# Kernel optimization log

Measured on AMD Instinct MI355X. Metric: run time of the kernel, lower is better.

## Reference

```python
import jax, jax.numpy as jnp
import numpy as np

H = 512   # hidden_size
E = 256   # embed_size / listener feature dim
V = 34    # vocab
EPS = 1e-12  # F.normalize(p=1) eps


def setup_inputs() -> dict:
    k = jax.random.key(0)
    ks = jax.random.split(k, 12)
    S, B, T = 512, 512, 160
    def n(kk, shape, s=0.05):
        return jax.random.normal(kk, shape, jnp.float32) * s
    return {
        "key": n(ks[0], (S, B, E), 1.0),
        "value": n(ks[1], (S, B, E), 1.0),
        "mask": jnp.ones((B, S), jnp.float32),
        "labels": jax.random.randint(ks[2], (B, T), 0, V),
        "Wq": n(ks[3], (E, H)), "bq": jnp.zeros((E,), jnp.float32),
        "Wsc": n(ks[4], (V, E + H)), "bsc": jnp.zeros((V,), jnp.float32),
        "Emb": n(ks[5], (V, E), 1.0),
        "Wih0": n(ks[6], (4 * H, H)), "Whh0": n(ks[7], (4 * H, H)),
        "bih0": jnp.zeros((4 * H,), jnp.float32), "bhh0": jnp.zeros((4 * H,), jnp.float32),
        "Wih1": n(ks[8], (4 * H, H)), "Whh1": n(ks[9], (4 * H, H)),
        "bih1": jnp.zeros((4 * H,), jnp.float32), "bhh1": jnp.zeros((4 * H,), jnp.float32),
        "s0": jnp.zeros((H,), jnp.float32), "s1": jnp.zeros((H,), jnp.float32),
        "cs0": jnp.zeros((H,), jnp.float32), "cs1": jnp.zeros((H,), jnp.float32),
    }


def _lstm_cell(x, h, c, Wih, Whh, bih, bhh):
    g = x @ Wih.T + bih + h @ Whh.T + bhh          # (B, 4H)
    i, f, gg, o = jnp.split(g, 4, axis=1)          # torch gate order i,f,g,o
    c2 = jax.nn.sigmoid(f) * c + jax.nn.sigmoid(i) * jnp.tanh(gg)
    h2 = jax.nn.sigmoid(o) * jnp.tanh(c2)
    return h2, c2


def reference(key, value, mask, labels, Wq, bq, Wsc, bsc, Emb,
              Wih0, Whh0, bih0, bhh0, Wih1, Whh1, bih1, bhh1,
              s0, s1, cs0, cs1):
    kT = jnp.transpose(key, (1, 0, 2))    # (B, S, E)
    vT = jnp.transpose(value, (1, 0, 2))  # (B, S, E)
    lab = labels.T                        # (T, B)
    embeds = Emb[lab]                     # (T, B, E)
    B = kT.shape[0]

    h0 = jnp.broadcast_to(s0, (B, H))
    h1 = jnp.broadcast_to(s1, (B, H))
    c0 = jnp.broadcast_to(cs0, (B, H))
    c1 = jnp.broadcast_to(cs1, (B, H))

    def attend(h):
        q = h @ Wq.T + bq                               # (B, E)
        e = jax.nn.softmax(jnp.einsum('bse,be->bs', kT, q), axis=1)
        e = e * mask
        alpha = e / jnp.maximum(jnp.sum(e, axis=1, keepdims=True), EPS)
        return jnp.einsum('bs,bse->be', alpha, vT)      # context (B, E)

    # step 0: attention + first cell updates, no scoring output
    ctx = attend(h1)
    inp = jnp.concatenate([embeds[0], ctx], axis=1)
    h0, c0 = _lstm_cell(inp, h0, c0, Wih0, Whh0, bih0, bhh0)
    h1, c1 = _lstm_cell(h0, h1, c1, Wih1, Whh1, bih1, bhh1)

    def step(carry, emb_i):
        h0, c0, h1, c1 = carry
        ctx = attend(h1)
        out = jnp.concatenate([h1, ctx], axis=1) @ Wsc.T + bsc  # (B, V)
        inp = jnp.concatenate([emb_i, ctx], axis=1)             # teacher forcing
        h0n, c0n = _lstm_cell(inp, h0, c0, Wih0, Whh0, bih0, bhh0)
        h1n, c1n = _lstm_cell(h0n, h1, c1, Wih1, Whh1, bih1, bhh1)
        return (h0n, c0n, h1n, c1n), out

    (h0, c0, h1, c1), outs = jax.lax.scan(step, (h0, c0, h1, c1), embeds[1:])

    ctx = attend(h1)
    out_last = jnp.concatenate([h1, ctx], axis=1) @ Wsc.T + bsc
    y = jnp.concatenate([outs, out_last[None]], axis=0)  # (T, B, V)
    return jnp.transpose(y, (1, 0, 2))                   # (B, T, V)
```

## Files before the change

kernel.cpp:

```cpp
#include <hip/hip_runtime.h>
#include <hip/hip_bf16.h>
#include <cstdint>
#include <cstddef>

#define S_LEN 512
#define B_SZ  512
#define T_LEN 160
#define E_DIM 256
#define H_DIM 512
#define V_DIM 34
#define G4    2048
#define XROW  768
#define EPS1  1e-12f
#define BE    (B_SZ * E_DIM)

typedef unsigned short u16;
typedef unsigned char  u8;
typedef __attribute__((ext_vector_type(8))) short bf16x8;
typedef __attribute__((ext_vector_type(4))) float f32x4;

#define SMEM_BYTES 18432

__device__ __forceinline__ float wave_reduce_sum(float v) {
#pragma unroll
  for (int m = 32; m >= 1; m >>= 1) v += __shfl_xor(v, m, 64);
  return v;
}
__device__ __forceinline__ float half_reduce_sum(float v) {
#pragma unroll
  for (int m = 16; m >= 1; m >>= 1) v += __shfl_xor(v, m, 64);
  return v;
}
__device__ __forceinline__ float wave_reduce_max(float v) {
#pragma unroll
  for (int m = 32; m >= 1; m >>= 1) v = fmaxf(v, __shfl_xor(v, m, 64));
  return v;
}
__device__ __forceinline__ float bf2f(u16 u) {
  return __uint_as_float((uint32_t)u << 16);
}
__device__ __forceinline__ float4 loadV4(const u8* p) {
  uint32_t u = *(const uint32_t*)p;
  float4 r;
  r.x = __builtin_amdgcn_cvt_f32_fp8(u, 0);
  r.y = __builtin_amdgcn_cvt_f32_fp8(u, 1);
  r.z = __builtin_amdgcn_cvt_f32_fp8(u, 2);
  r.w = __builtin_amdgcn_cvt_f32_fp8(u, 3);
  return r;
}
__device__ __forceinline__ float4 loadV4(const float* p) { return *(const float4*)p; }

__device__ __forceinline__ float dot8(const u16* p, const float* q) {
  bf16x8 k8 = *(const bf16x8*)p;
  float acc = 0.f;
#pragma unroll
  for (int i = 0; i < 8; ++i) acc += bf2f((u16)k8[i]) * q[i];
  return acc;
}
__device__ __forceinline__ float dot8(const float* p, const float* q) {
  float4 a = *(const float4*)p, b = *(const float4*)(p + 4);
  return a.x*q[0] + a.y*q[1] + a.z*q[2] + a.w*q[3] +
         b.x*q[4] + b.y*q[5] + b.z*q[6] + b.w*q[7];
}
__device__ __forceinline__ u16 f2bf(float f) {
  uint32_t u = __float_as_uint(f);
  uint32_t r = (u + 0x7FFFu + ((u >> 16) & 1u)) >> 16;
  return (u16)r;
}
__device__ __forceinline__ float sigm(float x) { return 1.f / (1.f + __expf(-x)); }

__device__ __forceinline__ void mfma_acc(const u16* A, int lda, const u16* W, int ldw,
                                         int klen, int m0, int n0, char* smem,
                                         f32x4 (&acc)[2][2]) {
  u16 (*As)[72] = (u16(*)[72])smem;
  u16 (*Ws)[72] = (u16(*)[72])(smem + 64 * 72 * 2);
  const int tid = threadIdx.x;
  const int lane = tid & 63, wave = tid >> 6;
  const int wm = (wave >> 1) * 32, wn = (wave & 1) * 32;
  const int row = lane & 15, kq = (lane >> 4) * 8;

  for (int k0 = 0; k0 < klen; k0 += 64) {
    __syncthreads();
#pragma unroll
    for (int i = tid; i < 512; i += 256) {
      int r = i >> 3, c = (i & 7) * 8;
      *(bf16x8*)&As[r][c] = *(const bf16x8*)(A + (size_t)(m0 + r) * lda + k0 + c);
      *(bf16x8*)&Ws[r][c] = *(const bf16x8*)(W + (size_t)(n0 + r) * ldw + k0 + c);
    }
    __syncthreads();
#pragma unroll
    for (int kk = 0; kk < 64; kk += 32) {
      bf16x8 a0 = *(const bf16x8*)&As[wm + row][kk + kq];
      bf16x8 a1 = *(const bf16x8*)&As[wm + 16 + row][kk + kq];
      bf16x8 b0 = *(const bf16x8*)&Ws[wn + row][kk + kq];
      bf16x8 b1 = *(const bf16x8*)&Ws[wn + 16 + row][kk + kq];
      acc[0][0] = __builtin_amdgcn_mfma_f32_16x16x32_bf16(a0, b0, acc[0][0], 0, 0, 0);
      acc[0][1] = __builtin_amdgcn_mfma_f32_16x16x32_bf16(a0, b1, acc[0][1], 0, 0, 0);
      acc[1][0] = __builtin_amdgcn_mfma_f32_16x16x32_bf16(a1, b0, acc[1][0], 0, 0, 0);
      acc[1][1] = __builtin_amdgcn_mfma_f32_16x16x32_bf16(a1, b1, acc[1][1], 0, 0, 0);
    }
  }
}

__global__ __launch_bounds__(256)
void init_state(const float* __restrict__ s0, const float* __restrict__ s1,
                const float* __restrict__ cs0, const float* __restrict__ cs1,
                u16* __restrict__ h0b, u16* __restrict__ h1b,
                float* __restrict__ c0, float* __restrict__ c1) {
  int idx = blockIdx.x * blockDim.x + threadIdx.x;
  int j = idx & 511;
  h0b[idx] = f2bf(s0[j]);
  h1b[idx] = f2bf(s1[j]);
  c0[idx] = cs0[j];
  c1[idx] = cs1[j];
}

__global__ __launch_bounds__(256)
void conv_bf16(const float* __restrict__ in, u16* __restrict__ outp, int n4) {
  int i = blockIdx.x * blockDim.x + threadIdx.x;
  int stride = gridDim.x * blockDim.x;
  for (; i < n4; i += stride) {
    float4 f = ((const float4*)in)[i];
    ushort4 u;
    u.x = f2bf(f.x); u.y = f2bf(f.y); u.z = f2bf(f.z); u.w = f2bf(f.w);
    ((ushort4*)outp)[i] = u;
  }
}

__global__ __launch_bounds__(256)
void conv_fp8(const float* __restrict__ in, u8* __restrict__ outp, int n4) {
  int i = blockIdx.x * blockDim.x + threadIdx.x;
  int stride = gridDim.x * blockDim.x;
  for (; i < n4; i += stride) {
    float4 f = ((const float4*)in)[i];
    uint32_t packed = 0;
    packed = __builtin_amdgcn_cvt_pk_fp8_f32(f.x, f.y, packed, false);
    packed = __builtin_amdgcn_cvt_pk_fp8_f32(f.z, f.w, packed, true);
    ((uint32_t*)outp)[i] = packed;
  }
}

__global__ __launch_bounds__(256)
void pack_w(const float* __restrict__ in, u16* __restrict__ outp) {
  int idx = blockIdx.x * 256 + threadIdx.x;
  int k = (idx & 63) * 8;
  int np = idx >> 6;
  int j = np >> 2, g = np & 3;
  const float* src = in + ((size_t)(g * 512 + j)) * 512 + k;
  float4 f0 = *(const float4*)src;
  float4 f1 = *(const float4*)(src + 4);
  ushort4 o0, o1;
  o0.x = f2bf(f0.x); o0.y = f2bf(f0.y); o0.z = f2bf(f0.z); o0.w = f2bf(f0.w);
  o1.x = f2bf(f1.x); o1.y = f2bf(f1.y); o1.z = f2bf(f1.z); o1.w = f2bf(f1.w);
  *(ushort4*)(outp + (size_t)np * 512 + k) = o0;
  *(ushort4*)(outp + (size_t)np * 512 + k + 4) = o1;
}

__global__ __launch_bounds__(256)
void pack_wq(const float* __restrict__ in, u16* __restrict__ outp) {
  int idx = blockIdx.x * 256 + threadIdx.x;
  int k = (idx & 63) * 8;
  int e = idx >> 6;
  const float* src = in + (size_t)e * 512 + k;
  float4 f0 = *(const float4*)src;
  float4 f1 = *(const float4*)(src + 4);
  ushort4 o0, o1;
  o0.x = f2bf(f0.x); o0.y = f2bf(f0.y); o0.z = f2bf(f0.z); o0.w = f2bf(f0.w);
  o1.x = f2bf(f1.x); o1.y = f2bf(f1.y); o1.z = f2bf(f1.z); o1.w = f2bf(f1.w);
  *(ushort4*)(outp + (size_t)e * 512 + k) = o0;
  *(ushort4*)(outp + (size_t)e * 512 + k + 4) = o1;
}

__global__ __launch_bounds__(256)
void pack_wsc(const float* __restrict__ in, u16* __restrict__ outp) {
  int idx = blockIdx.x * 256 + threadIdx.x;
  if (idx >= 64 * 96) return;
  int kq = (idx % 96) * 8;
  int v = idx / 96;
  ushort4 o0 = {0, 0, 0, 0}, o1 = {0, 0, 0, 0};
  if (v < V_DIM) {
    const float* src = in + (size_t)v * XROW + kq;
    float4 f0 = *(const float4*)src;
    float4 f1 = *(const float4*)(src + 4);
    o0.x = f2bf(f0.x); o0.y = f2bf(f0.y); o0.z = f2bf(f0.z); o0.w = f2bf(f0.w);
    o1.x = f2bf(f1.x); o1.y = f2bf(f1.y); o1.z = f2bf(f1.z); o1.w = f2bf(f1.w);
  }
  *(ushort4*)(outp + (size_t)v * XROW + kq) = o0;
  *(ushort4*)(outp + (size_t)v * XROW + kq + 4) = o1;
}

__global__ __launch_bounds__(256)
void pack_bias(const float* bih0, const float* bhh0,
               const float* bih1, const float* bhh1,
               float* bias0p, float* bias1p) {
  int np = blockIdx.x * 256 + threadIdx.x;
  int j = np >> 2, g = np & 3;
  int n = g * 512 + j;
  bias0p[np] = bih0[n] + bhh0[n];
  bias1p[np] = bih1[n] + bhh1[n];
}

__global__ __launch_bounds__(256)
void gather_embs(const float* __restrict__ Emb, const int* __restrict__ labels,
                 u16* __restrict__ embs) {
  int idx = blockIdx.x * 256 + threadIdx.x;
  if (idx >= T_LEN * B_SZ * 64) return;
  int q = idx & 63;
  int b = (idx >> 6) & 511;
  int t = idx >> 15;
  int lab = labels[(size_t)b * T_LEN + t];
  float4 f = *(const float4*)(Emb + (size_t)lab * E_DIM + q * 4);
  ushort4 o;
  o.x = f2bf(f.x); o.y = f2bf(f.y); o.z = f2bf(f.z); o.w = f2bf(f.w);
  *(ushort4*)(embs + ((size_t)t * B_SZ + b) * E_DIM + q * 4) = o;
}

__global__ __launch_bounds__(256)
void qgemm(const u16* __restrict__ h1b, const u16* __restrict__ Wqb,
           const float* __restrict__ bq, float* __restrict__ qbuf) {
  __shared__ char smem[SMEM_BYTES];
  const int lane = threadIdx.x & 63, wave = threadIdx.x >> 6;
  const int m0 = blockIdx.y * 64, n0 = blockIdx.x * 64;
  f32x4 acc[2][2] = {};
  mfma_acc(h1b, H_DIM, Wqb, 512, 512, m0, n0, smem, acc);
  const int wm = (wave >> 1) * 32, wn = (wave & 1) * 32;
  const int col = lane & 15, r4 = (lane >> 4) * 4;
#pragma unroll
  for (int fm = 0; fm < 2; ++fm)
#pragma unroll
    for (int fn = 0; fn < 2; ++fn) {
      int cc = n0 + wn + fn * 16 + col;
      float bias = bq[cc];
#pragma unroll
      for (int r = 0; r < 4; ++r) {
        int rr = m0 + wm + fm * 16 + r4 + r;
        qbuf[(size_t)rr * E_DIM + cc] = acc[fm][fn][r] + bias;
      }
    }
}

template <typename KT, typename VT, bool DEFER>
__global__ __launch_bounds__(256)
void fusedA(const KT* __restrict__ key, const VT* __restrict__ value,
            const float* __restrict__ mask, const float* __restrict__ qbuf,
            const float* __restrict__ Wsc, const float* __restrict__ bsc,
            const u16* __restrict__ embs,
            const u16* __restrict__ h0b, const u16* __restrict__ h1b,
            const u16* __restrict__ Wih0p, const u16* __restrict__ Whh0p,
            const u16* __restrict__ Whh1p,
            u16* __restrict__ xc0, u16* __restrict__ xhist,
            float* __restrict__ pg0, float* __restrict__ pg1,
            float* __restrict__ out, int t) {
  __shared__ char smem[SMEM_BYTES];
  const int tid = threadIdx.x;
  const int lane = tid & 63;
  const int wave = tid >> 6;

  if (blockIdx.x >= 512) {
    if (t >= T_LEN) return;
    int gb = blockIdx.x - 512;
    int m0 = ((gb & 255) >> 5) * 64, n0 = (gb & 31) * 64;
    f32x4 acc[2][2] = {};
    float* pg;
    if (gb < 256) {
      mfma_acc(h0b, H_DIM, Whh0p, 512, 512, m0, n0, smem, acc);
      mfma_acc(embs + (size_t)t * BE, E_DIM, Wih0p, 512, 256, m0, n0, smem, acc);
      pg = pg0;
    } else {
      mfma_acc(h1b, H_DIM, Whh1p, 512, 512, m0, n0, smem, acc);
      pg = pg1;
    }
    const int wm = (wave >> 1) * 32, wn = (wave & 1) * 32;
    const int col = lane & 15, r4 = (lane >> 4) * 4;
#pragma unroll
    for (int fm = 0; fm < 2; ++fm)
#pragma unroll
      for (int fn = 0; fn < 2; ++fn) {
        int cc = n0 + wn + fn * 16 + col;
#pragma unroll
        for (int r = 0; r < 4; ++r) {
          int rr = m0 + wm + fm * 16 + r4 + r;
          pg[(size_t)rr * G4 + cc] = acc[fm][fn][r];
        }
      }
    return;
  }

  float* qs   = (float*)smem;
  float* scb  = qs + 256;
  float* ctxs = scb + 512;
  float* ctxp = ctxs + 256;
  float* red  = ctxp + 1024;
  float* h1s  = red + 8;
  const int b = blockIdx.x;

  qs[tid] = qbuf[(size_t)b * E_DIM + tid];
  if (!DEFER) {
#pragma unroll
    for (int j = tid; j < H_DIM; j += 256) h1s[j] = bf2f(h1b[(size_t)b * H_DIM + j]);
  }
  __syncthreads();

  {
    int e0 = (lane & 31) << 3;
    float q8[8];
    *(float4*)&q8[0] = *(const float4*)&qs[e0];
    *(float4*)&q8[4] = *(const float4*)&qs[e0 + 4];
    int s = wave * 4 + (lane >> 5) * 2;
    const KT* kp = key + (size_t)s * BE + (size_t)b * E_DIM + e0;
#pragma unroll 4
    for (int it = 0; it < 32; ++it) {
      float a0 = dot8(kp, q8);
      float a1 = dot8(kp + BE, q8);
      a0 = half_reduce_sum(a0);
      a1 = half_reduce_sum(a1);
      if ((lane & 31) == 0) { scb[s] = a0; scb[s + 1] = a1; }
      s += 16;
      kp += (size_t)16 * BE;
    }
  }
  __syncthreads();

  float v0 = scb[tid], v1 = scb[tid + 256];
  {
    float lm = wave_reduce_max(fmaxf(v0, v1));
    if (lane == 0) red[wave] = lm;
  }
  __syncthreads();
  float smax = fmaxf(fmaxf(red[0], red[1]), fmaxf(red[2], red[3]));
  __syncthreads();
  float m0 = mask[(size_t)b * S_LEN + tid];
  float m1 = mask[(size_t)b * S_LEN + tid + 256];
  float p0 = __expf(v0 - smax), p1 = __expf(v1 - smax);
  float pm0 = p0 * m0, pm1 = p1 * m1;
  {
    float sP = wave_reduce_sum(p0 + p1);
    float sPM = wave_reduce_sum(pm0 + pm1);
    if (lane == 0) { red[wave] = sP; red[4 + wave] = sPM; }
  }
  __syncthreads();
  float P  = red[0] + red[1] + red[2] + red[3];
  float PM = red[4] + red[5] + red[6] + red[7];
  float inv = 1.f / fmaxf(PM, EPS1 * P);
  scb[tid] = pm0 * inv;
  scb[tid + 256] = pm1 * inv;
  __syncthreads();

  {
    float4 cacc = {0.f, 0.f, 0.f, 0.f};
    const VT* vp = value + (size_t)wave * BE + (size_t)b * E_DIM + (lane << 2);
#pragma unroll 16
    for (int s = wave; s < S_LEN; s += 4) {
      float a = scb[s];
      float4 v4 = loadV4(vp);
      cacc.x += a * v4.x; cacc.y += a * v4.y; cacc.z += a * v4.z; cacc.w += a * v4.w;
      vp += (size_t)4 * BE;
    }
    *(float4*)&ctxp[wave * 256 + (lane << 2)] = cacc;
  }
  __syncthreads();
  {
    float ctxe = ctxp[tid] + ctxp[256 + tid] + ctxp[512 + tid] + ctxp[768 + tid];
    ctxs[tid] = ctxe;
    u16 cb = f2bf(ctxe);
    if (t < T_LEN) xc0[(size_t)b * E_DIM + tid] = cb;
    if (DEFER && t >= 1) xhist[((size_t)t * B_SZ + b) * XROW + H_DIM + tid] = cb;
  }

  if (!DEFER) {
    __syncthreads();
    if (t >= 1) {
      for (int v = wave; v < V_DIM; v += 4) {
        const float4* wr = reinterpret_cast<const float4*>(Wsc + (size_t)v * XROW);
        float4 w0 = wr[lane];
        float4 w1 = wr[lane + 64];
        float4 w2 = wr[lane + 128];
        const float* ha = &h1s[4 * lane];
        const float* hb = &h1s[256 + 4 * lane];
        const float* cx = &ctxs[4 * lane];
        float acc = w0.x * ha[0] + w0.y * ha[1] + w0.z * ha[2] + w0.w * ha[3] +
                    w1.x * hb[0] + w1.y * hb[1] + w1.z * hb[2] + w1.w * hb[3] +
                    w2.x * cx[0] + w2.y * cx[1] + w2.z * cx[2] + w2.w * cx[3];
        acc = wave_reduce_sum(acc);
        if (lane == 0) out[((size_t)b * T_LEN + (t - 1)) * V_DIM + v] = acc + bsc[v];
      }
    }
  }
}

__global__ __launch_bounds__(256)
void cell_kernel(const u16* __restrict__ A, int lda, const u16* __restrict__ Wp,
                 int klen,
                 const float* __restrict__ pg, const float* __restrict__ biasp,
                 float* __restrict__ cbuf,
                 u16* __restrict__ hb, u16* __restrict__ xh) {
  __shared__ char smem[SMEM_BYTES];
  const int tid = threadIdx.x;
  const int lane = tid & 63, wave = tid >> 6;
  const int m0 = blockIdx.y * 64, n0 = blockIdx.x * 64;

  f32x4 acc[2][2] = {};
  mfma_acc(A, lda, Wp, 512, klen, m0, n0, smem, acc);
  __syncthreads();

  float (*Cs)[68] = (float(*)[68])smem;
  const int wm = (wave >> 1) * 32, wn = (wave & 1) * 32;
  const int col = lane & 15, r4 = (lane >> 4) * 4;
#pragma unroll
  for (int fm = 0; fm < 2; ++fm)
#pragma unroll
    for (int fn = 0; fn < 2; ++fn) {
      int cc = wn + fn * 16 + col;
      float bias = biasp[n0 + cc];
#pragma unroll
      for (int r = 0; r < 4; ++r) {
        int rr = wm + fm * 16 + r4 + r;
        Cs[rr][cc] = acc[fm][fn][r] + pg[(size_t)(m0 + rr) * G4 + n0 + cc] + bias;
      }
    }
  __syncthreads();

  for (int i = tid; i < 1024; i += 256) {
    int m = i >> 4, j = i & 15;
    float4 gv = *(const float4*)&Cs[m][j * 4];
    float ii = sigm(gv.x), ff = sigm(gv.y), tg = tanhf(gv.z), oo = sigm(gv.w);
    int gm = m0 + m, gj = (n0 >> 2) + j;
    size_t cidx = (size_t)gm * H_DIM + gj;
    float cn = ff * cbuf[cidx] + ii * tg;
    float hn = oo * tanhf(cn);
    cbuf[cidx] = cn;
    u16 hv = f2bf(hn);
    hb[cidx] = hv;
    if (xh) xh[(size_t)gm * XROW + gj] = hv;
  }
}

__global__ __launch_bounds__(256)
void score_kernel(const u16* __restrict__ xhist, const u16* __restrict__ Wscb,
                  const float* __restrict__ bsc, float* __restrict__ out) {
  __shared__ char smem[SMEM_BYTES];
  const int tau = blockIdx.x + 1;
  const int m0 = blockIdx.y * 64;
  const int lane = threadIdx.x & 63, wave = threadIdx.x >> 6;
  f32x4 acc[2][2] = {};
  mfma_acc(xhist + (size_t)tau * B_SZ * XROW, XROW, Wscb, XROW, XROW, m0, 0, smem, acc);
  const int wm = (wave >> 1) * 32, wn = (wave & 1) * 32;
  const int col = lane & 15, r4 = (lane >> 4) * 4;
#pragma unroll
  for (int fm = 0; fm < 2; ++fm)
#pragma unroll
    for (int fn = 0; fn < 2; ++fn) {
      int cc = wn + fn * 16 + col;
      if (cc >= V_DIM) continue;
      float bias = bsc[cc];
#pragma unroll
      for (int r = 0; r < 4; ++r) {
        int b = m0 + wm + fm * 16 + r4 + r;
        out[((size_t)b * T_LEN + (tau - 1)) * V_DIM + cc] = acc[fm][fn][r] + bias;
      }
    }
}

extern "C" void kernel_launch(void* const* d_in, const int* in_sizes, int n_in,
                              void* d_out, int out_size, void* d_ws, size_t ws_size,
                              hipStream_t stream) {
  (void)in_sizes; (void)n_in; (void)out_size;

  const float* key    = (const float*)d_in[0];
  const float* value  = (const float*)d_in[1];
  const float* mask   = (const float*)d_in[2];
  const int*   labels = (const int*)d_in[3];
  const float* Wq     = (const float*)d_in[4];
  const float* bq     = (const float*)d_in[5];
  const float* Wsc    = (const float*)d_in[6];
  const float* bsc    = (const float*)d_in[7];
  const float* Emb    = (const float*)d_in[8];
  const float* Wih0   = (const float*)d_in[9];
  const float* Whh0   = (const float*)d_in[10];
  const float* bih0   = (const float*)d_in[11];
  const float* bhh0   = (const float*)d_in[12];
  const float* Wih1   = (const float*)d_in[13];
  const float* Whh1   = (const float*)d_in[14];
  const float* bih1   = (const float*)d_in[15];
  const float* bhh1   = (const float*)d_in[16];
  const float* s0     = (const float*)d_in[17];
  const float* s1     = (const float*)d_in[18];
  const float* cs0    = (const float*)d_in[19];
  const float* cs1    = (const float*)d_in[20];
  float* out = (float*)d_out;

  char* ws = (char*)d_ws;
  size_t off = 0;
  auto alloc = [&](size_t bytes) -> void* {
    void* p = ws + off;
    off += (bytes + 255) & ~(size_t)255;
    return p;
  };
  u16*   h0b    = (u16*)alloc((size_t)B_SZ * H_DIM * 2);
  u16*   h1b    = (u16*)alloc((size_t)B_SZ * H_DIM * 2);
  float* c0     = (float*)alloc((size_t)B_SZ * H_DIM * 4);
  float* c1     = (float*)alloc((size_t)B_SZ * H_DIM * 4);
  u16*   xc0    = (u16*)alloc((size_t)B_SZ * E_DIM * 2);
  float* qbuf   = (float*)alloc((size_t)B_SZ * E_DIM * 4);
  float* pg0    = (float*)alloc((size_t)B_SZ * G4 * 4);
  float* pg1    = (float*)alloc((size_t)B_SZ * G4 * 4);
  u16*   Wih0p  = (u16*)alloc((size_t)G4 * 512 * 2);
  u16*   Whh0p  = (u16*)alloc((size_t)G4 * 512 * 2);
  u16*   Wih1p  = (u16*)alloc((size_t)G4 * 512 * 2);
  u16*   Whh1p  = (u16*)alloc((size_t)G4 * 512 * 2);
  u16*   Wqb    = (u16*)alloc((size_t)E_DIM * 512 * 2);
  u16*   Wscb   = (u16*)alloc((size_t)64 * XROW * 2);
  float* bias0p = (float*)alloc((size_t)G4 * 4);
  float* bias1p = (float*)alloc((size_t)G4 * 4);
  u16*   embs   = (u16*)alloc((size_t)T_LEN * B_SZ * E_DIM * 2);

  const size_t kv_elems = (size_t)S_LEN * B_SZ * E_DIM;
  bool lowkv = (ws_size >= off + kv_elems * 2 + kv_elems + 1024);
  u16* kb = nullptr; u8* vb = nullptr;
  if (lowkv) {
    kb = (u16*)alloc(kv_elems * 2);
    vb = (u8*)alloc(kv_elems);
  }
  const size_t xh_bytes = (size_t)(T_LEN + 1) * B_SZ * XROW * 2;
  bool defer = (ws_size >= off + xh_bytes + 1024);
  u16* xhist = nullptr;
  if (defer) xhist = (u16*)alloc(xh_bytes);

  init_state<<<(B_SZ * H_DIM) / 256, 256, 0, stream>>>(s0, s1, cs0, cs1, h0b, h1b, c0, c1);
  pack_w<<<512, 256, 0, stream>>>(Wih0, Wih0p);
  pack_w<<<512, 256, 0, stream>>>(Whh0, Whh0p);
  pack_w<<<512, 256, 0, stream>>>(Wih1, Wih1p);
  pack_w<<<512, 256, 0, stream>>>(Whh1, Whh1p);
  pack_wq<<<64, 256, 0, stream>>>(Wq, Wqb);
  if (defer) pack_wsc<<<24, 256, 0, stream>>>(Wsc, Wscb);
  pack_bias<<<8, 256, 0, stream>>>(bih0, bhh0, bih1, bhh1, bias0p, bias1p);
  gather_embs<<<(T_LEN * B_SZ * 64 + 255) / 256, 256, 0, stream>>>(Emb, labels, embs);

  if (lowkv) {
    int n4 = (int)(kv_elems / 4);
    conv_bf16<<<4096, 256, 0, stream>>>(key, kb, n4);
    conv_fp8<<<4096, 256, 0, stream>>>(value, vb, n4);
  }

  dim3 qgrid(E_DIM / 64, B_SZ / 64);
  qgemm<<<qgrid, 256, 0, stream>>>(h1b, Wqb, bq, qbuf);

  dim3 cell_grid(G4 / 64, B_SZ / 64);
  for (int t = 0; t <= T_LEN; ++t) {
    if (lowkv) {
      if (defer)
        fusedA<u16, u8, true><<<1024, 256, 0, stream>>>(
            kb, vb, mask, qbuf, Wsc, bsc, embs, h0b, h1b,
            Wih0p, Whh0p, Whh1p, xc0, xhist, pg0, pg1, out, t);
      else
        fusedA<u16, u8, false><<<1024, 256, 0, stream>>>(
            kb, vb, mask, qbuf, Wsc, bsc, embs, h0b, h1b,
            Wih0p, Whh0p, Whh1p, xc0, xhist, pg0, pg1, out, t);
    } else {
      if (defer)
        fusedA<float, float, true><<<1024, 256, 0, stream>>>(
            key, value, mask, qbuf, Wsc, bsc, embs, h0b, h1b,
            Wih0p, Whh0p, Whh1p, xc0, xhist, pg0, pg1, out, t);
      else
        fusedA<float, float, false><<<1024, 256, 0, stream>>>(
            key, value, mask, qbuf, Wsc, bsc, embs, h0b, h1b,
            Wih0p, Whh0p, Whh1p, xc0, xhist, pg0, pg1, out, t);
    }
    if (t < T_LEN) {
      cell_kernel<<<cell_grid, 256, 0, stream>>>(
          xc0, E_DIM, Wih0p + 256, 256, pg0, bias0p, c0, h0b, nullptr);
      cell_kernel<<<cell_grid, 256, 0, stream>>>(
          h0b, H_DIM, Wih1p, 512, pg1, bias1p, c1, h1b,
          defer ? xhist + (size_t)(t + 1) * B_SZ * XROW : nullptr);
      qgemm<<<qgrid, 256, 0, stream>>>(h1b, Wqb, bq, qbuf);
    }
  }

  if (defer) {
    dim3 sgrid(T_LEN, B_SZ / 64);
    score_kernel<<<sgrid, 256, 0, stream>>>(xhist, Wscb, bsc, out);
  }
}
```

Before: 10.86 ms.

## Load MFMA operands directly from global memory, dropping LDS staging and barriers

Replaces the shared-memory-tiled MFMA helper with one that loads bf16 fragments straight from global memory into registers, removing LDS stores and __syncthreads from every GEMM (qgemm, fusedA gate GEMMs, cell_kernel, score_kernel). Shared memory is now declared per kernel at its actual size, which may raise occupancy. The attention score loop is also restructured to process four sequence positions per iteration instead of two, for more loads in flight. The cost is that each wave now reads its operands from global memory or cache rather than sharing tiles through LDS, which raises L2 traffic and makes the loads less coalesced.

```diff
diff --git a/kernel.cpp b/kernel.cpp
--- a/kernel.cpp
+++ b/kernel.cpp
@@ -19,8 +19,6 @@
 typedef __attribute__((ext_vector_type(8))) short bf16x8;
 typedef __attribute__((ext_vector_type(4))) float f32x4;
 
-#define SMEM_BYTES 18432
-
 __device__ __forceinline__ float wave_reduce_sum(float v) {
 #pragma unroll
   for (int m = 32; m >= 1; m >>= 1) v += __shfl_xor(v, m, 64);
@@ -69,36 +67,26 @@
 }
 __device__ __forceinline__ float sigm(float x) { return 1.f / (1.f + __expf(-x)); }
 
-__device__ __forceinline__ void mfma_acc(const u16* A, int lda, const u16* W, int ldw,
-                                         int klen, int m0, int n0, char* smem,
-                                         f32x4 (&acc)[2][2]) {
-  u16 (*As)[72] = (u16(*)[72])smem;
-  u16 (*Ws)[72] = (u16(*)[72])(smem + 64 * 72 * 2);
-  const int tid = threadIdx.x;
-  const int lane = tid & 63, wave = tid >> 6;
+__device__ __forceinline__ void mfma_direct(const u16* A, int lda, const u16* W, int ldw,
+                                            int klen, int m0, int n0,
+                                            f32x4 (&acc)[2][2]) {
+  const int lane = threadIdx.x & 63, wave = threadIdx.x >> 6;
   const int wm = (wave >> 1) * 32, wn = (wave & 1) * 32;
   const int row = lane & 15, kq = (lane >> 4) * 8;
-
-  for (int k0 = 0; k0 < klen; k0 += 64) {
-    __syncthreads();
-#pragma unroll
-    for (int i = tid; i < 512; i += 256) {
-      int r = i >> 3, c = (i & 7) * 8;
-      *(bf16x8*)&As[r][c] = *(const bf16x8*)(A + (size_t)(m0 + r) * lda + k0 + c);
-      *(bf16x8*)&Ws[r][c] = *(const bf16x8*)(W + (size_t)(n0 + r) * ldw + k0 + c);
-    }
-    __syncthreads();
-#pragma unroll
-    for (int kk = 0; kk < 64; kk += 32) {
-      bf16x8 a0 = *(const bf16x8*)&As[wm + row][kk + kq];
-      bf16x8 a1 = *(const bf16x8*)&As[wm + 16 + row][kk + kq];
-      bf16x8 b0 = *(const bf16x8*)&Ws[wn + row][kk + kq];
-      bf16x8 b1 = *(const bf16x8*)&Ws[wn + 16 + row][kk + kq];
-      acc[0][0] = __builtin_amdgcn_mfma_f32_16x16x32_bf16(a0, b0, acc[0][0], 0, 0, 0);
-      acc[0][1] = __builtin_amdgcn_mfma_f32_16x16x32_bf16(a0, b1, acc[0][1], 0, 0, 0);
-      acc[1][0] = __builtin_amdgcn_mfma_f32_16x16x32_bf16(a1, b0, acc[1][0], 0, 0, 0);
-      acc[1][1] = __builtin_amdgcn_mfma_f32_16x16x32_bf16(a1, b1, acc[1][1], 0, 0, 0);
-    }
+  const u16* a0p = A + (size_t)(m0 + wm + row) * lda + kq;
+  const u16* a1p = A + (size_t)(m0 + wm + 16 + row) * lda + kq;
+  const u16* b0p = W + (size_t)(n0 + wn + row) * ldw + kq;
+  const u16* b1p = W + (size_t)(n0 + wn + 16 + row) * ldw + kq;
+#pragma unroll 4
+  for (int k = 0; k < klen; k += 32) {
+    bf16x8 a0 = *(const bf16x8*)(a0p + k);
+    bf16x8 a1 = *(const bf16x8*)(a1p + k);
+    bf16x8 b0 = *(const bf16x8*)(b0p + k);
+    bf16x8 b1 = *(const bf16x8*)(b1p + k);
+    acc[0][0] = __builtin_amdgcn_mfma_f32_16x16x32_bf16(a0, b0, acc[0][0], 0, 0, 0);
+    acc[0][1] = __builtin_amdgcn_mfma_f32_16x16x32_bf16(a0, b1, acc[0][1], 0, 0, 0);
+    acc[1][0] = __builtin_amdgcn_mfma_f32_16x16x32_bf16(a1, b0, acc[1][0], 0, 0, 0);
+    acc[1][1] = __builtin_amdgcn_mfma_f32_16x16x32_bf16(a1, b1, acc[1][1], 0, 0, 0);
   }
 }
 
@@ -218,11 +206,10 @@
 __global__ __launch_bounds__(256)
 void qgemm(const u16* __restrict__ h1b, const u16* __restrict__ Wqb,
            const float* __restrict__ bq, float* __restrict__ qbuf) {
-  __shared__ char smem[SMEM_BYTES];
   const int lane = threadIdx.x & 63, wave = threadIdx.x >> 6;
   const int m0 = blockIdx.y * 64, n0 = blockIdx.x * 64;
   f32x4 acc[2][2] = {};
-  mfma_acc(h1b, H_DIM, Wqb, 512, 512, m0, n0, smem, acc);
+  mfma_direct(h1b, H_DIM, Wqb, 512, 512, m0, n0, acc);
   const int wm = (wave >> 1) * 32, wn = (wave & 1) * 32;
   const int col = lane & 15, r4 = (lane >> 4) * 4;
 #pragma unroll
@@ -251,7 +238,12 @@
             u16* __restrict__ xc0, u16* __restrict__ xhist,
             float* __restrict__ pg0, float* __restrict__ pg1,
             float* __restrict__ out, int t) {
-  __shared__ char smem[SMEM_BYTES];
+  __shared__ float qs[256];
+  __shared__ float scb[512];
+  __shared__ float ctxs[256];
+  __shared__ float red[8];
+  __shared__ float h1s[512];
+  __shared__ float ctxp[1024];
   const int tid = threadIdx.x;
   const int lane = tid & 63;
   const int wave = tid >> 6;
@@ -263,11 +255,11 @@
     f32x4 acc[2][2] = {};
     float* pg;
     if (gb < 256) {
-      mfma_acc(h0b, H_DIM, Whh0p, 512, 512, m0, n0, smem, acc);
-      mfma_acc(embs + (size_t)t * BE, E_DIM, Wih0p, 512, 256, m0, n0, smem, acc);
+      mfma_direct(h0b, H_DIM, Whh0p, 512, 512, m0, n0, acc);
+      mfma_direct(embs + (size_t)t * BE, E_DIM, Wih0p, 512, 256, m0, n0, acc);
       pg = pg0;
     } else {
-      mfma_acc(h1b, H_DIM, Whh1p, 512, 512, m0, n0, smem, acc);
+      mfma_direct(h1b, H_DIM, Whh1p, 512, 512, m0, n0, acc);
       pg = pg1;
     }
     const int wm = (wave >> 1) * 32, wn = (wave & 1) * 32;
@@ -286,12 +278,6 @@
     return;
   }
 
-  float* qs   = (float*)smem;
-  float* scb  = qs + 256;
-  float* ctxs = scb + 512;
-  float* ctxp = ctxs + 256;
-  float* red  = ctxp + 1024;
-  float* h1s  = red + 8;
   const int b = blockIdx.x;
 
   qs[tid] = qbuf[(size_t)b * E_DIM + tid];
@@ -306,17 +292,21 @@
     float q8[8];
     *(float4*)&q8[0] = *(const float4*)&qs[e0];
     *(float4*)&q8[4] = *(const float4*)&qs[e0 + 4];
-    int s = wave * 4 + (lane >> 5) * 2;
+    int s = wave * 8 + (lane >> 5) * 4;
     const KT* kp = key + (size_t)s * BE + (size_t)b * E_DIM + e0;
-#pragma unroll 4
-    for (int it = 0; it < 32; ++it) {
+#pragma unroll 2
+    for (int it = 0; it < 16; ++it) {
       float a0 = dot8(kp, q8);
       float a1 = dot8(kp + BE, q8);
+      float a2 = dot8(kp + 2 * (size_t)BE, q8);
+      float a3 = dot8(kp + 3 * (size_t)BE, q8);
       a0 = half_reduce_sum(a0);
       a1 = half_reduce_sum(a1);
-      if ((lane & 31) == 0) { scb[s] = a0; scb[s + 1] = a1; }
-      s += 16;
-      kp += (size_t)16 * BE;
+      a2 = half_reduce_sum(a2);
+      a3 = half_reduce_sum(a3);
+      if ((lane & 31) == 0) { scb[s] = a0; scb[s + 1] = a1; scb[s + 2] = a2; scb[s + 3] = a3; }
+      s += 32;
+      kp += (size_t)32 * BE;
     }
   }
   __syncthreads();
@@ -394,16 +384,14 @@
                  const float* __restrict__ pg, const float* __restrict__ biasp,
                  float* __restrict__ cbuf,
                  u16* __restrict__ hb, u16* __restrict__ xh) {
-  __shared__ char smem[SMEM_BYTES];
+  __shared__ float Cs[64][68];
   const int tid = threadIdx.x;
   const int lane = tid & 63, wave = tid >> 6;
   const int m0 = blockIdx.y * 64, n0 = blockIdx.x * 64;
 
   f32x4 acc[2][2] = {};
-  mfma_acc(A, lda, Wp, 512, klen, m0, n0, smem, acc);
-  __syncthreads();
-
-  float (*Cs)[68] = (float(*)[68])smem;
+  mfma_direct(A, lda, Wp, 512, klen, m0, n0, acc);
+
   const int wm = (wave >> 1) * 32, wn = (wave & 1) * 32;
   const int col = lane & 15, r4 = (lane >> 4) * 4;
 #pragma unroll
@@ -438,12 +426,11 @@
 __global__ __launch_bounds__(256)
 void score_kernel(const u16* __restrict__ xhist, const u16* __restrict__ Wscb,
                   const float* __restrict__ bsc, float* __restrict__ out) {
-  __shared__ char smem[SMEM_BYTES];
   const int tau = blockIdx.x + 1;
   const int m0 = blockIdx.y * 64;
   const int lane = threadIdx.x & 63, wave = threadIdx.x >> 6;
   f32x4 acc[2][2] = {};
-  mfma_acc(xhist + (size_t)tau * B_SZ * XROW, XROW, Wscb, XROW, XROW, m0, 0, smem, acc);
+  mfma_direct(xhist + (size_t)tau * B_SZ * XROW, XROW, Wscb, XROW, XROW, m0, 0, acc);
   const int wm = (wave >> 1) * 32, wn = (wave & 1) * 32;
   const int col = lane & 15, r4 = (lane >> 4) * 4;
 #pragma unroll
```

Result: no change. 10.91 ms (median of 2 runs) (+0.5%).
